# Optimization experiments

Measured on AMD Instinct MI355X. Metric: run time of the kernel, lower is better.

The kernel has to match this reference:

```python
import jax, jax.numpy as jnp
import numpy as np

B, C_IN, H, W = 4, 256, 48, 48
HEADS, HD = 8, 64
N = H * W
SCALE = 1.0 / (HD ** 0.5)


def setup_inputs() -> dict:
    key = jax.random.key(0)
    ks = jax.random.split(key, 5)
    x = jax.random.normal(ks[0], (B, C_IN, H, W), dtype=jnp.float32)
    # 1x1 conv weights, squeezed: [heads, head_channels, in_channels]
    Wq = jax.random.normal(ks[1], (HEADS, HD, C_IN), dtype=jnp.float32) * (C_IN ** -0.5)
    Wk = jax.random.normal(ks[2], (HEADS, HD, C_IN), dtype=jnp.float32) * (C_IN ** -0.5)
    Wv = jax.random.normal(ks[3], (HEADS, HD, C_IN), dtype=jnp.float32) * (C_IN ** -0.5)
    # output 1x1 conv: [in_channels, heads*head_channels]
    Wo = jax.random.normal(ks[4], (C_IN, HEADS * HD), dtype=jnp.float32) * ((HEADS * HD) ** -0.5)
    return {"x": x, "Wq": Wq, "Wk": Wk, "Wv": Wv, "Wo": Wo}


def reference(x, Wq, Wk, Wv, Wo):
    b, c, h, w = x.shape
    n = h * w
    xf = x.reshape(b, c, n)  # [B, C, N]
    # per-head 1x1 convs == batched projections -> [heads, B, N, HD]
    q = jnp.einsum('hdc,bcn->hbnd', Wq, xf)
    k = jnp.einsum('hdc,bcn->hbnd', Wk, xf)
    v = jnp.einsum('hdc,bcn->hbnd', Wv, xf)
    scores = jnp.einsum('hbnd,hbmd->hbnm', q, k) * SCALE  # [heads, B, N, N]
    probs = jax.nn.softmax(scores, axis=-1)
    ws = jnp.einsum('hbnm,hbmd->hbnd', probs, v)  # [heads, B, N, HD]
    # faithful replication of torch: transpose(1,2) then reshape(B, heads*HD, H, W)
    ws = jnp.transpose(ws, (0, 2, 1, 3))  # [heads, N, B, HD]
    ws = ws.reshape(b, HEADS * HD, h, w)
    out = jnp.einsum('oc,bchw->bohw', Wo, ws)  # output 1x1 conv
    return out
```

## Files before the change

### kernel.cpp

```cpp
#include <hip/hip_runtime.h>

#define B_     4
#define CIN    256
#define NTOK   2304
#define HEADS  8
#define HD     64
#define SCALE  0.125f
#define LOG2E  1.44269504088896f
#define QSCALE (SCALE * LOG2E)
#define PBIAS  4.0f
#define QKV_ELEMS (HEADS * B_ * NTOK * HD)
#define HBSTRIDE 147456
#define WSZ    131072

typedef _Float16 f16;
typedef _Float16 __attribute__((ext_vector_type(8))) h8v;
typedef _Float16 __attribute__((ext_vector_type(4))) h4v;
typedef ushort   __attribute__((ext_vector_type(8))) us8;
typedef float    __attribute__((ext_vector_type(16))) f16v;

__device__ inline uint pk2(float a, float b) {
    auto v = __builtin_amdgcn_cvt_pkrtz(a, b);
    return __builtin_bit_cast(uint, v);
}
#define EXP2(x) __builtin_amdgcn_exp2f(x)

#define GLOAD_LDS(g, l) __builtin_amdgcn_global_load_lds( \
    (const __attribute__((address_space(1))) unsigned int*)(g), \
    (__attribute__((address_space(3))) unsigned int*)(l), 16, 0, 0)

__global__ __launch_bounds__(256) void castw(
    const float* __restrict__ Wq, const float* __restrict__ Wk,
    const float* __restrict__ Wv, const float* __restrict__ Wo,
    f16* __restrict__ wc, f16* __restrict__ woc)
{
    int e4 = (blockIdx.x * 256 + threadIdx.x) * 4;
    const float* src; f16* dst; float mult = 1.0f; int off;
    if (e4 < WSZ)          { src = Wq; off = e4;           dst = wc;           mult = QSCALE; }
    else if (e4 < 2 * WSZ) { src = Wk; off = e4 - WSZ;     dst = wc + WSZ; }
    else if (e4 < 3 * WSZ) { src = Wv; off = e4 - 2 * WSZ; dst = wc + 2 * WSZ; }
    else                   { src = Wo; off = e4 - 3 * WSZ; dst = woc; }
    float4 r = *(const float4*)(src + off);
    h4v hv;
    hv.x = (f16)(r.x * mult); hv.y = (f16)(r.y * mult);
    hv.z = (f16)(r.z * mult); hv.w = (f16)(r.w * mult);
    *(h4v*)(dst + off) = hv;
}

__global__ __launch_bounds__(256) void tcastf(
    const float* __restrict__ src, f16* __restrict__ dst, int C)
{
    const int n0 = blockIdx.x * 64;
    const int c0 = blockIdx.y * 64;
    const int b  = blockIdx.z;
    __shared__ float T[64][65];
    const int tid = threadIdx.x;
    const float* sb = src + ((size_t)b * C + c0) * NTOK;
    #pragma unroll
    for (int i = 0; i < 16; ++i) {
        int idx = tid + 256 * i;
        int rr = idx >> 6, ll = idx & 63;
        T[ll][rr] = sb[(size_t)rr * NTOK + n0 + ll];
    }
    __syncthreads();
    const size_t ob = ((size_t)b * NTOK + n0) * C + c0;
    #pragma unroll
    for (int i = 0; i < 4; ++i) {
        int idx = tid + 256 * i;
        int row = idx >> 4, c4 = (idx & 15) * 4;
        h4v v;
        v.x = (f16)T[row][c4 + 0]; v.y = (f16)T[row][c4 + 1];
        v.z = (f16)T[row][c4 + 2]; v.w = (f16)T[row][c4 + 3];
        *(h4v*)(dst + ob + (size_t)row * C + c4) = v;
    }
}

__global__ __launch_bounds__(128) void proj_mfma(
    const f16* __restrict__ wc, const f16* __restrict__ xt,
    f16* __restrict__ qh, f16* __restrict__ kh, f16* __restrict__ vth)
{
    const int ntile = blockIdx.x;
    const int hp    = blockIdx.y;
    const int b     = blockIdx.z;
    const int p     = hp >> 3, h = hp & 7;
    const int hb    = h * 4 + b;
    const f16* Wp = wc + ((size_t)p * 8 + h) * (HD * CIN);

    __shared__ __align__(16) f16 Ws[2][64][64], Xs[2][64][64];

    const int tid = threadIdx.x;
    const int w = tid >> 6, lane = tid & 63;
    const int lm = lane & 31, lh = lane >> 5;
    const int n_loc  = w * 32 + lm;
    const int n_glob = ntile * 64 + n_loc;

    const f16* xb = xt + ((size_t)b * NTOK + ntile * 64) * CIN;

    auto stage = [&](int buf, int c0) {
        const f16* src = (w == 0) ? Wp : xb;
        f16* dst = (w == 0) ? &Ws[buf][0][0] : &Xs[buf][0][0];
        #pragma unroll
        for (int i = 0; i < 8; ++i) {
            int g = i * 64 + lane; int row = g >> 3; int c = (g & 7) ^ (row & 7);
            GLOAD_LDS(src + (size_t)row * CIN + c0 + c * 8, dst + i * 512);
        }
    };

    f16v o0, o1;
    #pragma unroll
    for (int i = 0; i < 16; ++i) { o0[i] = 0.f; o1[i] = 0.f; }

    stage(0, 0);
    for (int c0 = 0; c0 < CIN; c0 += 64) {
        const int cur = (c0 >> 6) & 1;
        __syncthreads();
        if (c0 + 64 < CIN) stage(cur ^ 1, c0 + 64);
        #pragma unroll
        for (int s = 0; s < 4; ++s) {
            const int pp = ((2 * s + lh) ^ (lm & 7)) * 8;
            h8v a0 = *(const h8v*)&Ws[cur][lm][pp];
            h8v a1 = *(const h8v*)&Ws[cur][lm + 32][pp];
            h8v bh = *(const h8v*)&Xs[cur][n_loc][pp];
            o0 = __builtin_amdgcn_mfma_f32_32x32x16_f16(a0, bh, o0, 0, 0, 0);
            o1 = __builtin_amdgcn_mfma_f32_32x32x16_f16(a1, bh, o1, 0, 0, 0);
        }
    }

    const size_t hboff = (size_t)hb * HBSTRIDE;
    if (p < 2) {
        f16* oh = ((p == 0) ? qh : kh) + hboff + (size_t)n_glob * 64;
        #pragma unroll
        for (int t = 0; t < 2; ++t) {
            const f16v& oc = t ? o1 : o0;
            #pragma unroll
            for (int g = 0; g < 4; ++g) {
                int d0 = 8 * g + 4 * lh + 32 * t;
                h4v hv;
                hv.x = (f16)oc[4 * g + 0]; hv.y = (f16)oc[4 * g + 1];
                hv.z = (f16)oc[4 * g + 2]; hv.w = (f16)oc[4 * g + 3];
                *(h4v*)(oh + d0) = hv;
            }
        }
    } else {
        f16* oh = vth + hboff;
        #pragma unroll
        for (int t = 0; t < 2; ++t) {
            const f16v& oc = t ? o1 : o0;
            #pragma unroll
            for (int r = 0; r < 16; ++r) {
                int d = (r & 3) + 8 * (r >> 2) + 4 * lh + 32 * t;
                oh[(size_t)d * NTOK + n_glob] = (f16)oc[r];
            }
        }
    }
}

__global__ __launch_bounds__(256, 2) void attn_mfma(
    const f16* __restrict__ qh, const f16* __restrict__ kh,
    const f16* __restrict__ vth, f16* __restrict__ wsth)
{
    const int bid   = blockIdx.x;
    const int xcd   = bid & 7;
    const int slot  = bid >> 3;
    const int hb    = xcd * 4 + (slot / 36);
    const int rtile = slot % 36;
    const int h_    = hb >> 2, b = hb & 3;
    const int tid   = threadIdx.x;
    const int w     = tid >> 6;
    const int lane  = tid & 63;
    const int lm    = lane & 31;
    const int lh    = lane >> 5;
    const int rh    = w & 1;
    const int ks    = w >> 1;

    __shared__ __align__(16) f16 SMEM[2][2][2][64][64];

    const size_t hboff = (size_t)hb * HBSTRIDE;
    const int m = rtile * 64 + rh * 32 + lm;

    h8v Qf[4];
    #pragma unroll
    for (int s = 0; s < 4; ++s)
        Qf[s] = *(const h8v*)(qh + hboff + (size_t)m * 64 + (2 * s + lh) * 8);

    f16v o0, o1;
    #pragma unroll
    for (int i = 0; i < 16; ++i) { o0[i] = 0.f; o1[i] = 0.f; }
    float lsum = 0.f;

    const int  sv  = w >> 1;
    const int  stp = w & 1;
    const f16* gb  = (sv == 0) ? kh + hboff : vth + hboff;

    auto stage = [&](int buf, int st) {
        const int kts = 2 * st + stp;
        f16* dst = &SMEM[buf][sv][stp][0][0];
        #pragma unroll
        for (int i = 0; i < 8; ++i) {
            int g   = i * 64 + lane;
            int row = g >> 3;
            int c   = (g & 7) ^ (row & 7);
            const f16* src = (sv == 0)
                ? gb + kts * 4096 + row * 64 + c * 8
                : gb + (size_t)row * 2304 + kts * 64 + c * 8;
            GLOAD_LDS(src, dst + i * 512);
        }
    };

    stage(0, 0);
    __syncthreads();

    for (int st = 0; st < 18; ++st) {
        const int cur = st & 1;
        if (st + 1 < 18) stage(cur ^ 1, st + 1);

        f16v s0, s1;
        #pragma unroll
        for (int i = 0; i < 16; ++i) { s0[i] = -PBIAS; s1[i] = -PBIAS; }

        __builtin_amdgcn_s_setprio(1);
        #pragma unroll
        for (int s = 0; s < 4; ++s) {
            const int p = ((2 * s + lh) ^ (lm & 7)) * 8;
            h8v k0 = *(const h8v*)&SMEM[cur][0][ks][lm][p];
            h8v k1 = *(const h8v*)&SMEM[cur][0][ks][lm + 32][p];
            s0 = __builtin_amdgcn_mfma_f32_32x32x16_f16(k0, Qf[s], s0, 0, 0, 0);
            s1 = __builtin_amdgcn_mfma_f32_32x32x16_f16(k1, Qf[s], s1, 0, 0, 0);
        }
        __builtin_amdgcn_s_setprio(0);

        float rs = 0.f;
        #pragma unroll
        for (int i = 0; i < 16; ++i) { s0[i] = EXP2(s0[i]); rs += s0[i]; }
        #pragma unroll
        for (int i = 0; i < 16; ++i) { s1[i] = EXP2(s1[i]); rs += s1[i]; }
        lsum += rs;

        uint Ppk[2][8];
        #pragma unroll
        for (int pr = 0; pr < 8; ++pr) {
            Ppk[0][pr] = pk2(s0[2 * pr], s0[2 * pr + 1]);
            Ppk[1][pr] = pk2(s1[2 * pr], s1[2 * pr + 1]);
        }

        h8v pf[4];
        #pragma unroll
        for (int s = 0; s < 4; ++s) {
            const int jt = s >> 1, q = 4 * (s & 1);
            uint kp0 = lh ? Ppk[jt][q + 2] : Ppk[jt][q + 0];
            uint kp1 = lh ? Ppk[jt][q + 3] : Ppk[jt][q + 1];
            uint sp0 = lh ? Ppk[jt][q + 0] : Ppk[jt][q + 2];
            uint sp1 = lh ? Ppk[jt][q + 1] : Ppk[jt][q + 3];
            uint rp0 = (uint)__shfl_xor((int)sp0, 32);
            uint rp1 = (uint)__shfl_xor((int)sp1, 32);
            uint4 u = { lh ? rp0 : kp0, lh ? rp1 : kp1,
                        lh ? kp0 : rp0, lh ? kp1 : rp1 };
            pf[s] = __builtin_bit_cast(h8v, u);
        }

        __builtin_amdgcn_s_setprio(1);
        #pragma unroll
        for (int s = 0; s < 4; ++s) {
            const int p = ((2 * s + lh) ^ (lm & 7)) * 8;
            h8v v0 = *(const h8v*)&SMEM[cur][1][ks][lm][p];
            h8v v1 = *(const h8v*)&SMEM[cur][1][ks][lm + 32][p];
            o0 = __builtin_amdgcn_mfma_f32_32x32x16_f16(v0, pf[s], o0, 0, 0, 0);
            o1 = __builtin_amdgcn_mfma_f32_32x32x16_f16(v1, pf[s], o1, 0, 0, 0);
        }
        __builtin_amdgcn_s_setprio(0);

        __syncthreads();
    }

    float* red = (float*)&SMEM[0][0][0][0][0];
    if (ks == 1) {
        float* dst = red + (size_t)(rh * 64 + lane) * 33;
        #pragma unroll
        for (int i = 0; i < 16; ++i) { dst[i] = o0[i]; dst[16 + i] = o1[i]; }
        dst[32] = lsum;
    }
    __syncthreads();
    if (ks == 0) {
        const float* sp = red + (size_t)(rh * 64 + lane) * 33;
        #pragma unroll
        for (int i = 0; i < 16; ++i) { o0[i] += sp[i]; o1[i] += sp[16 + i]; }
        lsum += sp[32];
        lsum += __shfl_xor(lsum, 32);
        float inv = 1.0f / lsum;
        f16* wrow = wsth + ((size_t)h_ * NTOK + m) * 256 + b * 64;
        #pragma unroll
        for (int g = 0; g < 4; ++g) {
            h4v r0, r1;
            r0.x = (f16)(o0[4 * g + 0] * inv); r0.y = (f16)(o0[4 * g + 1] * inv);
            r0.z = (f16)(o0[4 * g + 2] * inv); r0.w = (f16)(o0[4 * g + 3] * inv);
            *(h4v*)(wrow + 8 * g + 4 * lh) = r0;
            r1.x = (f16)(o1[4 * g + 0] * inv); r1.y = (f16)(o1[4 * g + 1] * inv);
            r1.z = (f16)(o1[4 * g + 2] * inv); r1.w = (f16)(o1[4 * g + 3] * inv);
            *(h4v*)(wrow + 32 + 8 * g + 4 * lh) = r1;
        }
    }
}

__global__ __launch_bounds__(128) void outconv_mfma(
    const f16* __restrict__ woc, const f16* __restrict__ ws,
    float* __restrict__ out)
{
    const int ntile = blockIdx.x;
    const int otile = blockIdx.y;
    const int b     = blockIdx.z;

    __shared__ __align__(16) f16 Wos[2][64][64];
    __shared__ __align__(16) f16 Xs[2][64][72];

    const int tid = threadIdx.x;
    const int w = tid >> 6, lane = tid & 63;
    const int lm = lane & 31, lh = lane >> 5;
    const int n_loc  = w * 32 + lm;
    const int n_glob = ntile * 64 + n_loc;
    const int pr = tid >> 2;
    const int qn = tid & 3;

    const f16* Wb = woc + (size_t)(otile * 64) * 512;
    const f16* wsb = ws + (size_t)b * 512 * NTOK + ntile * 64 + qn * 16;

    auto stageW = [&](int buf, int c0) {
        #pragma unroll
        for (int j = 0; j < 4; ++j) {
            int i = w * 4 + j;
            int g = i * 64 + lane; int row = g >> 3; int c = (g & 7) ^ (row & 7);
            GLOAD_LDS(Wb + (size_t)row * 512 + c0 + c * 8,
                      &Wos[buf][0][0] + i * 512);
        }
    };

    uint4 x0, x1, x2, x3;
    auto loadB = [&](int c0) {
        const f16* r0 = wsb + (size_t)(c0 + 2 * pr) * NTOK;
        const f16* r1 = r0 + NTOK;
        x0 = *(const uint4*)(r0);
        x1 = *(const uint4*)(r0 + 8);
        x2 = *(const uint4*)(r1);
        x3 = *(const uint4*)(r1 + 8);
    };
    auto storeB = [&](int buf) {
        us8 a0 = __builtin_bit_cast(us8, x0), a1 = __builtin_bit_cast(us8, x1);
        us8 b0 = __builtin_bit_cast(us8, x2), b1 = __builtin_bit_cast(us8, x3);
        #pragma unroll
        for (int j = 0; j < 8; ++j) {
            *(uint*)&Xs[buf][qn * 16 + j][2 * pr]     = (uint)a0[j] | ((uint)b0[j] << 16);
            *(uint*)&Xs[buf][qn * 16 + 8 + j][2 * pr] = (uint)a1[j] | ((uint)b1[j] << 16);
        }
    };

    f16v o0, o1;
    #pragma unroll
    for (int i = 0; i < 16; ++i) { o0[i] = 0.f; o1[i] = 0.f; }

    stageW(0, 0);
    loadB(0);
    storeB(0);
    for (int c0 = 0; c0 < 512; c0 += 64) {
        const int cur = (c0 >> 6) & 1;
        __syncthreads();
        if (c0 + 64 < 512) { stageW(cur ^ 1, c0 + 64); loadB(c0 + 64); }
        #pragma unroll
        for (int s = 0; s < 4; ++s) {
            const int pp = ((2 * s + lh) ^ (lm & 7)) * 8;
            const int co = (2 * s + lh) * 8;
            h8v a0 = *(const h8v*)&Wos[cur][lm][pp];
            h8v a1 = *(const h8v*)&Wos[cur][lm + 32][pp];
            h8v bh = *(const h8v*)&Xs[cur][n_loc][co];
            o0 = __builtin_amdgcn_mfma_f32_32x32x16_f16(a0, bh, o0, 0, 0, 0);
            o1 = __builtin_amdgcn_mfma_f32_32x32x16_f16(a1, bh, o1, 0, 0, 0);
        }
        if (c0 + 64 < 512) storeB(cur ^ 1);
    }

    #pragma unroll
    for (int t = 0; t < 2; ++t) {
        const f16v& oc = t ? o1 : o0;
        #pragma unroll
        for (int r = 0; r < 16; ++r) {
            int orow = otile * 64 + (r & 3) + 8 * (r >> 2) + 4 * lh + 32 * t;
            out[((size_t)b * CIN + orow) * NTOK + n_glob] = oc[r];
        }
    }
}

extern "C" void kernel_launch(void* const* d_in, const int* in_sizes, int n_in,
                              void* d_out, int out_size, void* d_ws, size_t ws_size,
                              hipStream_t stream)
{
    const float* x  = (const float*)d_in[0];
    const float* Wq = (const float*)d_in[1];
    const float* Wk = (const float*)d_in[2];
    const float* Wv = (const float*)d_in[3];
    const float* Wo = (const float*)d_in[4];
    float* out = (float*)d_out;

    f16* qh   = (f16*)d_ws;
    f16* kh   = qh   + QKV_ELEMS;
    f16* vth  = kh   + QKV_ELEMS;
    f16* wsth = vth  + QKV_ELEMS;
    f16* xt   = wsth;
    f16* wc   = wsth + QKV_ELEMS;
    f16* woc  = wc   + 3 * WSZ;

    castw<<<dim3(512), 256, 0, stream>>>(Wq, Wk, Wv, Wo, wc, woc);
    tcastf<<<dim3(36, 4, 4), 256, 0, stream>>>(x, xt, CIN);
    proj_mfma<<<dim3(36, 24, 4), 128, 0, stream>>>(wc, xt, qh, kh, vth);
    attn_mfma<<<dim3(1152), 256, 0, stream>>>(qh, kh, vth, wsth);
    outconv_mfma<<<dim3(36, 4, 4), 128, 0, stream>>>(woc, wsth, out);
}
```

Measured before the change: 177.4 us.

## Load K/V fragments directly from global memory instead of LDS double-buffering

Removes the shared-memory staging pipeline for K and V tiles: each wave now loads its MFMA operand fragments straight from global memory into registers and drops the per-iteration barrier. LDS use shrinks to a small reduction buffer, and launch bounds are raised to allow four blocks per CU. The aim is to remove LDS traffic and synchronization stalls and to raise occupancy. In exchange, the two waves sharing a K/V tile each fetch it separately through the caches. There is no software prefetch, so global latency sits on the critical path, and the V loads stride by NTOK per row.

Result: slower. 335.9 us (+89.3%).

```diff
diff --git a/kernel.cpp b/kernel.cpp
--- a/kernel.cpp
+++ b/kernel.cpp
@@ -155,7 +155,7 @@
     }
 }
 
-__global__ __launch_bounds__(256, 2) void attn_mfma(
+__global__ __launch_bounds__(256, 4) void attn_mfma(
     const f16* __restrict__ qh, const f16* __restrict__ kh,
     const f16* __restrict__ vth, f16* __restrict__ wsth)
 {
@@ -173,7 +173,7 @@
     const int rh    = w & 1;
     const int ks    = w >> 1;
 
-    __shared__ __align__(16) f16 SMEM[2][2][2][64][64];
+    __shared__ float RED[128][33];
 
     const size_t hboff = (size_t)hb * HBSTRIDE;
     const int m = rtile * 64 + rh * 32 + lm;
@@ -188,31 +188,19 @@
     for (int i = 0; i < 16; ++i) { o0[i] = 0.f; o1[i] = 0.f; }
     float lsum = 0.f;
 
-    const int  sv  = w >> 1;
-    const int  stp = w & 1;
-    const f16* gb  = (sv == 0) ? kh + hboff : vth + hboff;
-
-    auto stage = [&](int buf, int st) {
-        const int kts = 2 * st + stp;
-        f16* dst = &SMEM[buf][sv][stp][0][0];
-        #pragma unroll
-        for (int i = 0; i < 8; ++i) {
-            int g   = i * 64 + lane;
-            int row = g >> 3;
-            int c   = (g & 7) ^ (row & 7);
-            const f16* src = (sv == 0)
-                ? gb + kts * 4096 + row * 64 + c * 8
-                : gb + (size_t)row * 2304 + kts * 64 + c * 8;
-            GLOAD_LDS(src, dst + i * 512);
-        }
-    };
-
-    stage(0, 0);
-    __syncthreads();
+    const f16* kb0 = kh + hboff;
+    const f16* vb0 = vth + hboff;
 
     for (int st = 0; st < 18; ++st) {
-        const int cur = st & 1;
-        if (st + 1 < 18) stage(cur ^ 1, st + 1);
+        const int kt = 2 * st + ks;
+
+        const f16* kb = kb0 + (size_t)kt * 4096;
+        h8v kf0[4], kf1[4];
+        #pragma unroll
+        for (int s = 0; s < 4; ++s) {
+            kf0[s] = *(const h8v*)(kb + lm * 64 + (2 * s + lh) * 8);
+            kf1[s] = *(const h8v*)(kb + (lm + 32) * 64 + (2 * s + lh) * 8);
+        }
 
         f16v s0, s1;
         #pragma unroll
@@ -221,11 +209,8 @@
         __builtin_amdgcn_s_setprio(1);
         #pragma unroll
         for (int s = 0; s < 4; ++s) {
-            const int p = ((2 * s + lh) ^ (lm & 7)) * 8;
-            h8v k0 = *(const h8v*)&SMEM[cur][0][ks][lm][p];
-            h8v k1 = *(const h8v*)&SMEM[cur][0][ks][lm + 32][p];
-            s0 = __builtin_amdgcn_mfma_f32_32x32x16_f16(k0, Qf[s], s0, 0, 0, 0);
-            s1 = __builtin_amdgcn_mfma_f32_32x32x16_f16(k1, Qf[s], s1, 0, 0, 0);
+            s0 = __builtin_amdgcn_mfma_f32_32x32x16_f16(kf0[s], Qf[s], s0, 0, 0, 0);
+            s1 = __builtin_amdgcn_mfma_f32_32x32x16_f16(kf1[s], Qf[s], s1, 0, 0, 0);
         }
         __builtin_amdgcn_s_setprio(0);
 
@@ -241,6 +226,14 @@
         for (int pr = 0; pr < 8; ++pr) {
             Ppk[0][pr] = pk2(s0[2 * pr], s0[2 * pr + 1]);
             Ppk[1][pr] = pk2(s1[2 * pr], s1[2 * pr + 1]);
+        }
+
+        const f16* vb = vb0 + kt * 64;
+        h8v vf0[4], vf1[4];
+        #pragma unroll
+        for (int s = 0; s < 4; ++s) {
+            vf0[s] = *(const h8v*)(vb + (size_t)lm * NTOK + (2 * s + lh) * 8);
+            vf1[s] = *(const h8v*)(vb + (size_t)(lm + 32) * NTOK + (2 * s + lh) * 8);
         }
 
         h8v pf[4];
@@ -261,18 +254,13 @@
         __builtin_amdgcn_s_setprio(1);
         #pragma unroll
         for (int s = 0; s < 4; ++s) {
-            const int p = ((2 * s + lh) ^ (lm & 7)) * 8;
-            h8v v0 = *(const h8v*)&SMEM[cur][1][ks][lm][p];
-            h8v v1 = *(const h8v*)&SMEM[cur][1][ks][lm + 32][p];
-            o0 = __builtin_amdgcn_mfma_f32_32x32x16_f16(v0, pf[s], o0, 0, 0, 0);
-            o1 = __builtin_amdgcn_mfma_f32_32x32x16_f16(v1, pf[s], o1, 0, 0, 0);
+            o0 = __builtin_amdgcn_mfma_f32_32x32x16_f16(vf0[s], pf[s], o0, 0, 0, 0);
+            o1 = __builtin_amdgcn_mfma_f32_32x32x16_f16(vf1[s], pf[s], o1, 0, 0, 0);
         }
         __builtin_amdgcn_s_setprio(0);
-
-        __syncthreads();
-    }
-
-    float* red = (float*)&SMEM[0][0][0][0][0];
+    }
+
+    float* red = &RED[0][0];
     if (ks == 1) {
         float* dst = red + (size_t)(rh * 64 + lane) * 33;
         #pragma unroll
```

## Process two query tiles per warp in attention and swap shuffles for permlane32

Applied to the files above, without the earlier changes.

Each attention block now covers 128 query rows instead of 64, so every warp handles two 32-row query groups (A and B). The K and V fragments loaded from shared memory are reused across both groups, which halves the K/V staging traffic per query and halves the grid to 576 blocks. The P-fragment exchange between half-waves now uses permlane32_swap in place of shfl_xor plus selects. The cost is roughly double the accumulator and score registers per thread, which may lower occupancy under launch_bounds(256,2), and fewer blocks to spread across the CUs.

Result: faster. 172.6 us (-2.7%).

```diff
diff --git a/kernel.cpp b/kernel.cpp
--- a/kernel.cpp
+++ b/kernel.cpp
@@ -162,31 +162,34 @@
     const int bid   = blockIdx.x;
     const int xcd   = bid & 7;
     const int slot  = bid >> 3;
-    const int hb    = xcd * 4 + (slot / 36);
-    const int rtile = slot % 36;
+    const int hb    = xcd * 4 + (slot / 18);
+    const int rpair = slot % 18;
     const int h_    = hb >> 2, b = hb & 3;
     const int tid   = threadIdx.x;
     const int w     = tid >> 6;
     const int lane  = tid & 63;
     const int lm    = lane & 31;
     const int lh    = lane >> 5;
-    const int rh    = w & 1;
-    const int ks    = w >> 1;
+    const int qg    = w >> 1;
+    const int ks    = w & 1;
 
     __shared__ __align__(16) f16 SMEM[2][2][2][64][64];
 
     const size_t hboff = (size_t)hb * HBSTRIDE;
-    const int m = rtile * 64 + rh * 32 + lm;
-
-    h8v Qf[4];
-    #pragma unroll
-    for (int s = 0; s < 4; ++s)
-        Qf[s] = *(const h8v*)(qh + hboff + (size_t)m * 64 + (2 * s + lh) * 8);
-
-    f16v o0, o1;
-    #pragma unroll
-    for (int i = 0; i < 16; ++i) { o0[i] = 0.f; o1[i] = 0.f; }
-    float lsum = 0.f;
+    const int mA = rpair * 128 + qg * 64 + lm;
+    const int mB = mA + 32;
+
+    h8v QfA[4], QfB[4];
+    #pragma unroll
+    for (int s = 0; s < 4; ++s) {
+        QfA[s] = *(const h8v*)(qh + hboff + (size_t)mA * 64 + (2 * s + lh) * 8);
+        QfB[s] = *(const h8v*)(qh + hboff + (size_t)mB * 64 + (2 * s + lh) * 8);
+    }
+
+    f16v oA0, oA1, oB0, oB1;
+    #pragma unroll
+    for (int i = 0; i < 16; ++i) { oA0[i] = 0.f; oA1[i] = 0.f; oB0[i] = 0.f; oB1[i] = 0.f; }
+    float lsumA = 0.f, lsumB = 0.f;
 
     const int  sv  = w >> 1;
     const int  stp = w & 1;
@@ -214,9 +217,11 @@
         const int cur = st & 1;
         if (st + 1 < 18) stage(cur ^ 1, st + 1);
 
-        f16v s0, s1;
-        #pragma unroll
-        for (int i = 0; i < 16; ++i) { s0[i] = -PBIAS; s1[i] = -PBIAS; }
+        f16v sA0, sA1, sB0, sB1;
+        #pragma unroll
+        for (int i = 0; i < 16; ++i) {
+            sA0[i] = -PBIAS; sA1[i] = -PBIAS; sB0[i] = -PBIAS; sB1[i] = -PBIAS;
+        }
 
         __builtin_amdgcn_s_setprio(1);
         #pragma unroll
@@ -224,38 +229,49 @@
             const int p = ((2 * s + lh) ^ (lm & 7)) * 8;
             h8v k0 = *(const h8v*)&SMEM[cur][0][ks][lm][p];
             h8v k1 = *(const h8v*)&SMEM[cur][0][ks][lm + 32][p];
-            s0 = __builtin_amdgcn_mfma_f32_32x32x16_f16(k0, Qf[s], s0, 0, 0, 0);
-            s1 = __builtin_amdgcn_mfma_f32_32x32x16_f16(k1, Qf[s], s1, 0, 0, 0);
+            sA0 = __builtin_amdgcn_mfma_f32_32x32x16_f16(k0, QfA[s], sA0, 0, 0, 0);
+            sA1 = __builtin_amdgcn_mfma_f32_32x32x16_f16(k1, QfA[s], sA1, 0, 0, 0);
+            sB0 = __builtin_amdgcn_mfma_f32_32x32x16_f16(k0, QfB[s], sB0, 0, 0, 0);
+            sB1 = __builtin_amdgcn_mfma_f32_32x32x16_f16(k1, QfB[s], sB1, 0, 0, 0);
         }
         __builtin_amdgcn_s_setprio(0);
 
-        float rs = 0.f;
-        #pragma unroll
-        for (int i = 0; i < 16; ++i) { s0[i] = EXP2(s0[i]); rs += s0[i]; }
-        #pragma unroll
-        for (int i = 0; i < 16; ++i) { s1[i] = EXP2(s1[i]); rs += s1[i]; }
-        lsum += rs;
-
-        uint Ppk[2][8];
+        float rsA = 0.f, rsB = 0.f;
+        #pragma unroll
+        for (int i = 0; i < 16; ++i) { sA0[i] = EXP2(sA0[i]); rsA += sA0[i]; }
+        #pragma unroll
+        for (int i = 0; i < 16; ++i) { sA1[i] = EXP2(sA1[i]); rsA += sA1[i]; }
+        #pragma unroll
+        for (int i = 0; i < 16; ++i) { sB0[i] = EXP2(sB0[i]); rsB += sB0[i]; }
+        #pragma unroll
+        for (int i = 0; i < 16; ++i) { sB1[i] = EXP2(sB1[i]); rsB += sB1[i]; }
+        lsumA += rsA; lsumB += rsB;
+
+        uint PpkA[2][8], PpkB[2][8];
         #pragma unroll
         for (int pr = 0; pr < 8; ++pr) {
-            Ppk[0][pr] = pk2(s0[2 * pr], s0[2 * pr + 1]);
-            Ppk[1][pr] = pk2(s1[2 * pr], s1[2 * pr + 1]);
-        }
-
-        h8v pf[4];
+            PpkA[0][pr] = pk2(sA0[2 * pr], sA0[2 * pr + 1]);
+            PpkA[1][pr] = pk2(sA1[2 * pr], sA1[2 * pr + 1]);
+            PpkB[0][pr] = pk2(sB0[2 * pr], sB0[2 * pr + 1]);
+            PpkB[1][pr] = pk2(sB1[2 * pr], sB1[2 * pr + 1]);
+        }
+
+        h8v pfA[4], pfB[4];
         #pragma unroll
         for (int s = 0; s < 4; ++s) {
             const int jt = s >> 1, q = 4 * (s & 1);
-            uint kp0 = lh ? Ppk[jt][q + 2] : Ppk[jt][q + 0];
-            uint kp1 = lh ? Ppk[jt][q + 3] : Ppk[jt][q + 1];
-            uint sp0 = lh ? Ppk[jt][q + 0] : Ppk[jt][q + 2];
-            uint sp1 = lh ? Ppk[jt][q + 1] : Ppk[jt][q + 3];
-            uint rp0 = (uint)__shfl_xor((int)sp0, 32);
-            uint rp1 = (uint)__shfl_xor((int)sp1, 32);
-            uint4 u = { lh ? rp0 : kp0, lh ? rp1 : kp1,
-                        lh ? kp0 : rp0, lh ? kp1 : rp1 };
-            pf[s] = __builtin_bit_cast(h8v, u);
+            auto a02 = __builtin_amdgcn_permlane32_swap(
+                PpkA[jt][q + 0], PpkA[jt][q + 2], false, false);
+            auto a13 = __builtin_amdgcn_permlane32_swap(
+                PpkA[jt][q + 1], PpkA[jt][q + 3], false, false);
+            uint4 ua = { a02[0], a13[0], a02[1], a13[1] };
+            pfA[s] = __builtin_bit_cast(h8v, ua);
+            auto b02 = __builtin_amdgcn_permlane32_swap(
+                PpkB[jt][q + 0], PpkB[jt][q + 2], false, false);
+            auto b13 = __builtin_amdgcn_permlane32_swap(
+                PpkB[jt][q + 1], PpkB[jt][q + 3], false, false);
+            uint4 ub = { b02[0], b13[0], b02[1], b13[1] };
+            pfB[s] = __builtin_bit_cast(h8v, ub);
         }
 
         __builtin_amdgcn_s_setprio(1);
@@ -264,8 +280,10 @@
             const int p = ((2 * s + lh) ^ (lm & 7)) * 8;
             h8v v0 = *(const h8v*)&SMEM[cur][1][ks][lm][p];
             h8v v1 = *(const h8v*)&SMEM[cur][1][ks][lm + 32][p];
-            o0 = __builtin_amdgcn_mfma_f32_32x32x16_f16(v0, pf[s], o0, 0, 0, 0);
-            o1 = __builtin_amdgcn_mfma_f32_32x32x16_f16(v1, pf[s], o1, 0, 0, 0);
+            oA0 = __builtin_amdgcn_mfma_f32_32x32x16_f16(v0, pfA[s], oA0, 0, 0, 0);
+            oA1 = __builtin_amdgcn_mfma_f32_32x32x16_f16(v1, pfA[s], oA1, 0, 0, 0);
+            oB0 = __builtin_amdgcn_mfma_f32_32x32x16_f16(v0, pfB[s], oB0, 0, 0, 0);
+            oB1 = __builtin_amdgcn_mfma_f32_32x32x16_f16(v1, pfB[s], oB1, 0, 0, 0);
         }
         __builtin_amdgcn_s_setprio(0);
 
@@ -274,29 +292,50 @@
 
     float* red = (float*)&SMEM[0][0][0][0][0];
     if (ks == 1) {
-        float* dst = red + (size_t)(rh * 64 + lane) * 33;
-        #pragma unroll
-        for (int i = 0; i < 16; ++i) { dst[i] = o0[i]; dst[16 + i] = o1[i]; }
-        dst[32] = lsum;
+        float* dA = red + (size_t)(qg * 128 + lane) * 33;
+        float* dB = red + (size_t)(qg * 128 + 64 + lane) * 33;
+        #pragma unroll
+        for (int i = 0; i < 16; ++i) {
+            dA[i] = oA0[i]; dA[16 + i] = oA1[i];
+            dB[i] = oB0[i]; dB[16 + i] = oB1[i];
+        }
+        dA[32] = lsumA; dB[32] = lsumB;
     }
     __syncthreads();
     if (ks == 0) {
-        const float* sp = red + (size_t)(rh * 64 + lane) * 33;
-        #pragma unroll
-        for (int i = 0; i < 16; ++i) { o0[i] += sp[i]; o1[i] += sp[16 + i]; }
-        lsum += sp[32];
-        lsum += __shfl_xor(lsum, 32);
-        float inv = 1.0f / lsum;
-        f16* wrow = wsth + ((size_t)h_ * NTOK + m) * 256 + b * 64;
+        const float* sA = red + (size_t)(qg * 128 + lane) * 33;
+        const float* sB = red + (size_t)(qg * 128 + 64 + lane) * 33;
+        #pragma unroll
+        for (int i = 0; i < 16; ++i) {
+            oA0[i] += sA[i]; oA1[i] += sA[16 + i];
+            oB0[i] += sB[i]; oB1[i] += sB[16 + i];
+        }
+        lsumA += sA[32]; lsumB += sB[32];
+        lsumA += __shfl_xor(lsumA, 32);
+        lsumB += __shfl_xor(lsumB, 32);
+        float invA = 1.0f / lsumA, invB = 1.0f / lsumB;
+
+        f16* wrA = wsth + ((size_t)h_ * NTOK + mA) * 256 + b * 64;
+        f16* wrB = wsth + ((size_t)h_ * NTOK + mB) * 256 + b * 64;
         #pragma unroll
         for (int g = 0; g < 4; ++g) {
             h4v r0, r1;
-            r0.x = (f16)(o0[4 * g + 0] * inv); r0.y = (f16)(o0[4 * g + 1] * inv);
-            r0.z = (f16)(o0[4 * g + 2] * inv); r0.w = (f16)(o0[4 * g + 3] * inv);
-            *(h4v*)(wrow + 8 * g + 4 * lh) = r0;
-            r1.x = (f16)(o1[4 * g + 0] * inv); r1.y = (f16)(o1[4 * g + 1] * inv);
-            r1.z = (f16)(o1[4 * g + 2] * inv); r1.w = (f16)(o1[4 * g + 3] * inv);
-            *(h4v*)(wrow + 32 + 8 * g + 4 * lh) = r1;
+            r0.x = (f16)(oA0[4 * g + 0] * invA); r0.y = (f16)(oA0[4 * g + 1] * invA);
+            r0.z = (f16)(oA0[4 * g + 2] * invA); r0.w = (f16)(oA0[4 * g + 3] * invA);
+            *(h4v*)(wrA + 8 * g + 4 * lh) = r0;
+            r1.x = (f16)(oA1[4 * g + 0] * invA); r1.y = (f16)(oA1[4 * g + 1] * invA);
+            r1.z = (f16)(oA1[4 * g + 2] * invA); r1.w = (f16)(oA1[4 * g + 3] * invA);
+            *(h4v*)(wrA + 32 + 8 * g + 4 * lh) = r1;
+        }
+        #pragma unroll
+        for (int g = 0; g < 4; ++g) {
+            h4v r0, r1;
+            r0.x = (f16)(oB0[4 * g + 0] * invB); r0.y = (f16)(oB0[4 * g + 1] * invB);
+            r0.z = (f16)(oB0[4 * g + 2] * invB); r0.w = (f16)(oB0[4 * g + 3] * invB);
+            *(h4v*)(wrB + 8 * g + 4 * lh) = r0;
+            r1.x = (f16)(oB1[4 * g + 0] * invB); r1.y = (f16)(oB1[4 * g + 1] * invB);
+            r1.z = (f16)(oB1[4 * g + 2] * invB); r1.w = (f16)(oB1[4 * g + 3] * invB);
+            *(h4v*)(wrB + 32 + 8 * g + 4 * lh) = r1;
         }
     }
 }
@@ -409,6 +448,6 @@
     castw<<<dim3(512), 256, 0, stream>>>(Wq, Wk, Wv, Wo, wc, woc);
     tcastf<<<dim3(36, 4, 4), 256, 0, stream>>>(x, xt, CIN);
     proj_mfma<<<dim3(36, 24, 4), 128, 0, stream>>>(wc, xt, qh, kh, vth);
-    attn_mfma<<<dim3(1152), 256, 0, stream>>>(qh, kh, vth, wsth);
+    attn_mfma<<<dim3(576), 256, 0, stream>>>(qh, kh, vth, wsth);
     outconv_mfma<<<dim3(36, 4, 4), 128, 0, stream>>>(woc, wsth, out);
 }
```
